# Kernel optimization log

Hardware: AMD Instinct MI355X
Metric: run time of the kernel (lower is better)

The kernel has to match this reference:

```python
import jax, jax.numpy as jnp
import numpy as np

N = 50000      # nodes
E = 800000     # edges
G = 1024       # graphs in batch
D_IN = 9       # atom feature dim
D = 64         # embedding_size


def _lin(k, fan_in, shape):
    s = 1.0 / np.sqrt(fan_in)
    return jax.random.uniform(k, shape, jnp.float32, -s, s)


def setup_inputs() -> dict:
    key = jax.random.key(0)
    ks = jax.random.split(key, 12)
    x = jax.random.normal(ks[0], (N, D_IN), dtype=jnp.float32)
    edge_index = jax.random.randint(ks[1], (2, E), 0, N, dtype=jnp.int32)
    # node -> graph id, sorted, every graph non-empty
    batch = (jnp.arange(N) * G // N).astype(jnp.int32)
    W0 = _lin(ks[2], D_IN, (D_IN, D)); b0 = _lin(ks[3], D_IN, (D,))
    W1 = _lin(ks[4], D, (D, D));       b1 = _lin(ks[5], D, (D,))
    W2 = _lin(ks[6], D, (D, D));       b2 = _lin(ks[7], D, (D,))
    W3 = _lin(ks[8], D, (D, D));       b3 = _lin(ks[9], D, (D,))
    Wout = _lin(ks[10], 2 * D, (2 * D, 1)); bout = _lin(ks[11], 2 * D, (1,))
    return {"x": x, "edge_index": edge_index, "batch": batch,
            "W0": W0, "b0": b0, "W1": W1, "b1": b1,
            "W2": W2, "b2": b2, "W3": W3, "b3": b3,
            "Wout": Wout, "bout": bout}


def reference(x, edge_index, batch, W0, b0, W1, b1, W2, b2, W3, b3, Wout, bout):
    n = x.shape[0]
    # GCNConv: add self-loops, symmetric normalization D^-1/2 (A+I) D^-1/2
    loops = jnp.arange(n, dtype=edge_index.dtype)
    row = jnp.concatenate([edge_index[0], loops])  # source
    col = jnp.concatenate([edge_index[1], loops])  # destination
    deg = jax.ops.segment_sum(jnp.ones_like(col, dtype=x.dtype), col, num_segments=n)
    dinv = jax.lax.rsqrt(deg)  # deg >= 1 thanks to self-loops
    norm = dinv[row] * dinv[col]  # [E+N]

    def conv(h, W, b):
        h = h @ W                               # [N, D]
        msg = norm[:, None] * h[row]            # [E+N, D]
        return jax.ops.segment_sum(msg, col, num_segments=n) + b

    h = jnp.tanh(conv(x, W0, b0))
    h = jnp.tanh(conv(h, W1, b1))
    h = jnp.tanh(conv(h, W2, b2))
    h = jnp.tanh(conv(h, W3, b3))
    # dropout is identity in eval mode
    gmax = jax.ops.segment_max(h, batch, num_segments=G)                       # [G, D]
    cnt = jax.ops.segment_sum(jnp.ones((n, 1), h.dtype), batch, num_segments=G)
    gmean = jax.ops.segment_sum(h, batch, num_segments=G) / jnp.maximum(cnt, 1.0)
    pooled = jnp.concatenate([gmax, gmean], axis=1)                            # [G, 2D]
    return pooled @ Wout + bout
```

## Files before the change

### kernel.cpp

```cpp
#include <hip/hip_runtime.h>
#include <hip/hip_fp16.h>
#include <math.h>

#define N_NODES 50000
#define N_EDGES 800000
#define N_GRAPHS 1024
#define DIM 64
#define PAD 64
#define ZROW N_NODES


__global__ void deg_fill(const int* __restrict__ row, const int* __restrict__ col,
                         int* __restrict__ ideg, int* __restrict__ esrc_pad) {
    int e = blockIdx.x * 256 + threadIdx.x;
    if (e >= N_EDGES) return;
    int r = row[e];
    int c = col[e];
    int rank = atomicAdd(&ideg[c], 1);
    if (rank < PAD) esrc_pad[c * PAD + rank] = r;
}


__global__ void gemm9(const float* __restrict__ x, const float* __restrict__ W,
                      const int* __restrict__ ideg, __half* __restrict__ th) {
    __shared__ float Wl[9 * DIM];
    int tid = threadIdx.x;
    for (int i = tid; i < 9 * DIM; i += 256) Wl[i] = W[i];
    __syncthreads();
    int node = blockIdx.x * 4 + (tid >> 6);
    int d = tid & 63;
    if (node >= N_NODES) return;
    const float* xr = x + (size_t)node * 9;
    float acc = 0.0f;
#pragma unroll
    for (int k = 0; k < 9; ++k) acc += xr[k] * Wl[k * DIM + d];
    float dv = rsqrtf((float)ideg[node] + 1.0f);
    th[(size_t)node * DIM + d] = __float2half(dv * acc);
}

__global__ void gemm64(const float* __restrict__ h, const float* __restrict__ W,
                       const int* __restrict__ ideg, uint2* __restrict__ th2) {
    __shared__ float At[64][68];
    __shared__ float Bl[64][68];
    int tid = threadIdx.x;
    int n0 = blockIdx.x * 64;

    {
        const float4* W4 = (const float4*)W;
#pragma unroll
        for (int i = 0; i < 4; ++i) {
            int idx = tid + 256 * i;
            int k = idx >> 4;
            int d4 = idx & 15;
            float4 v = W4[idx];
            *(float4*)&Bl[k][d4 * 4] = v;
        }
    }
    {
        int node = tid >> 2;
        int seg = tid & 3;
        int gn = n0 + node;
        bool ok = gn < N_NODES;
        const float4* h4 = (const float4*)h;
#pragma unroll
        for (int i = 0; i < 4; ++i) {
            int c4 = seg * 4 + i;
            float4 v = ok ? h4[(size_t)gn * 16 + c4] : make_float4(0.f, 0.f, 0.f, 0.f);
            int d = c4 * 4;
            At[d + 0][node] = v.x;
            At[d + 1][node] = v.y;
            At[d + 2][node] = v.z;
            At[d + 3][node] = v.w;
        }
    }
    __syncthreads();

    int ty = tid >> 4;
    int tx = tid & 15;
    float c00 = 0, c01 = 0, c02 = 0, c03 = 0;
    float c10 = 0, c11 = 0, c12 = 0, c13 = 0;
    float c20 = 0, c21 = 0, c22 = 0, c23 = 0;
    float c30 = 0, c31 = 0, c32 = 0, c33 = 0;
#pragma unroll 8
    for (int k = 0; k < 64; ++k) {
        float4 a = *(const float4*)&At[k][ty * 4];
        float4 b = *(const float4*)&Bl[k][tx * 4];
        c00 += a.x * b.x; c01 += a.x * b.y; c02 += a.x * b.z; c03 += a.x * b.w;
        c10 += a.y * b.x; c11 += a.y * b.y; c12 += a.y * b.z; c13 += a.y * b.w;
        c20 += a.z * b.x; c21 += a.z * b.y; c22 += a.z * b.z; c23 += a.z * b.w;
        c30 += a.w * b.x; c31 += a.w * b.y; c32 += a.w * b.z; c33 += a.w * b.w;
    }
    int gn = n0 + ty * 4;
#define STORE_ROW(r, CA, CB, CC, CD)                                          \
    if (gn + r < N_NODES) {                                                   \
        float dv = rsqrtf((float)ideg[gn + r] + 1.0f);                        \
        __half2 p0 = __floats2half2_rn(dv * CA, dv * CB);                     \
        __half2 p1 = __floats2half2_rn(dv * CC, dv * CD);                     \
        uint2 o;                                                              \
        o.x = *(unsigned*)&p0;                                                \
        o.y = *(unsigned*)&p1;                                                \
        th2[(size_t)(gn + r) * 16 + tx] = o;                                  \
    }
    STORE_ROW(0, c00, c01, c02, c03)
    STORE_ROW(1, c10, c11, c12, c13)
    STORE_ROW(2, c20, c21, c22, c23)
    STORE_ROW(3, c30, c31, c32, c33)
#undef STORE_ROW
}


__device__ __forceinline__ float4 h4tof4(uint2 v) {
    __half2 a = *reinterpret_cast<const __half2*>(&v.x);
    __half2 c = *reinterpret_cast<const __half2*>(&v.y);
    float2 fa = __half22float2(a);
    float2 fc = __half22float2(c);
    return make_float4(fa.x, fa.y, fc.x, fc.y);
}

__device__ __forceinline__ void add4(float4& a, const float4& r) {
    a.x += r.x; a.y += r.y; a.z += r.z; a.w += r.w;
}

__device__ __forceinline__ void fold4(float4& a, int m) {
    a.x += __shfl_xor(a.x, m, 64);
    a.y += __shfl_xor(a.y, m, 64);
    a.z += __shfl_xor(a.z, m, 64);
    a.w += __shfl_xor(a.w, m, 64);
}

__global__ void gather_tanh(const int* __restrict__ esrc_pad, const int* __restrict__ ideg,
                            const uint2* __restrict__ th2, const float* __restrict__ b,
                            float4* __restrict__ hout4) {
    int tid = threadIdx.x;
    int wid = tid >> 6;
    int lane = tid & 63;
    int sub = lane & 15;
    int grp = lane >> 4;
    int nodeA = blockIdx.x * 8 + wid * 2;
    int nodeB = nodeA + 1;

    int degA = min(ideg[nodeA], PAD);
    int degB = min(ideg[nodeB], PAD);
    int sA = nodeA * PAD, sB = nodeB * PAD;
    int eA = sA + degA, eB = sB + degB;

    float4 accA = make_float4(0.f, 0.f, 0.f, 0.f);
    float4 accB = make_float4(0.f, 0.f, 0.f, 0.f);

    if (grp == 0) add4(accA, h4tof4(th2[(size_t)nodeA * 16 + sub]));
    else if (grp == 1) add4(accB, h4tof4(th2[(size_t)nodeB * 16 + sub]));

    int iters = max((degA + 15) >> 4, (degB + 15) >> 4);
    int jA = sA + grp, jB = sB + grp;

    for (int it = 0; it < iters; ++it) {
        bool vA0 = jA + 0 < eA, vA1 = jA + 4 < eA, vA2 = jA + 8 < eA, vA3 = jA + 12 < eA;
        bool vB0 = jB + 0 < eB, vB1 = jB + 4 < eB, vB2 = jB + 8 < eB, vB3 = jB + 12 < eB;
        int a0 = esrc_pad[vA0 ? jA + 0 : 0], a1 = esrc_pad[vA1 ? jA + 4 : 0];
        int a2 = esrc_pad[vA2 ? jA + 8 : 0], a3 = esrc_pad[vA3 ? jA + 12 : 0];
        int b0 = esrc_pad[vB0 ? jB + 0 : 0], b1 = esrc_pad[vB1 ? jB + 4 : 0];
        int b2 = esrc_pad[vB2 ? jB + 8 : 0], b3 = esrc_pad[vB3 ? jB + 12 : 0];
        a0 = vA0 ? a0 : ZROW; a1 = vA1 ? a1 : ZROW; a2 = vA2 ? a2 : ZROW; a3 = vA3 ? a3 : ZROW;
        b0 = vB0 ? b0 : ZROW; b1 = vB1 ? b1 : ZROW; b2 = vB2 ? b2 : ZROW; b3 = vB3 ? b3 : ZROW;
        uint2 rA0 = th2[(size_t)a0 * 16 + sub];
        uint2 rA1 = th2[(size_t)a1 * 16 + sub];
        uint2 rA2 = th2[(size_t)a2 * 16 + sub];
        uint2 rA3 = th2[(size_t)a3 * 16 + sub];
        uint2 rB0 = th2[(size_t)b0 * 16 + sub];
        uint2 rB1 = th2[(size_t)b1 * 16 + sub];
        uint2 rB2 = th2[(size_t)b2 * 16 + sub];
        uint2 rB3 = th2[(size_t)b3 * 16 + sub];
        add4(accA, h4tof4(rA0)); add4(accA, h4tof4(rA1));
        add4(accA, h4tof4(rA2)); add4(accA, h4tof4(rA3));
        add4(accB, h4tof4(rB0)); add4(accB, h4tof4(rB1));
        add4(accB, h4tof4(rB2)); add4(accB, h4tof4(rB3));
        jA += 16; jB += 16;
    }

    fold4(accA, 16);
    fold4(accA, 32);
    fold4(accB, 16);
    fold4(accB, 32);

    float4 bv = ((const float4*)b)[sub];
    float dvA = rsqrtf((float)degA + 1.0f);
    float dvB = rsqrtf((float)degB + 1.0f);
    float dv = (grp == 1) ? dvB : dvA;
    float4 res = (grp == 1) ? accB : accA;
    res.x = tanhf(dv * res.x + bv.x);
    res.y = tanhf(dv * res.y + bv.y);
    res.z = tanhf(dv * res.z + bv.z);
    res.w = tanhf(dv * res.w + bv.w);
    if (grp == 0) hout4[(size_t)nodeA * 16 + sub] = res;
    else if (grp == 1) hout4[(size_t)nodeB * 16 + sub] = res;
}


__device__ __forceinline__ int lower_bound(const int* a, int n, int key) {
    int lo = 0, hi = n;
    while (lo < hi) {
        int mid = (lo + hi) >> 1;
        if (a[mid] < key) lo = mid + 1; else hi = mid;
    }
    return lo;
}

__global__ void pool_out(const float* __restrict__ h, const int* __restrict__ batch,
                         const float* __restrict__ Wout, const float* __restrict__ bout,
                         float* __restrict__ out) {
    __shared__ float smax[4][DIM];
    __shared__ float ssum[4][DIM];
    __shared__ int bounds[2];
    int g = blockIdx.x;
    int tid = threadIdx.x, w = tid >> 6, d = tid & 63;
    if (tid == 0) {
        bounds[0] = lower_bound(batch, N_NODES, g);
        bounds[1] = lower_bound(batch, N_NODES, g + 1);
    }
    __syncthreads();
    int start = bounds[0], end = bounds[1];
    float mx = -INFINITY, sum = 0.0f;
    for (int n = start + w; n < end; n += 4) {
        float v = h[(size_t)n * DIM + d];
        mx = fmaxf(mx, v);
        sum += v;
    }
    smax[w][d] = mx;
    ssum[w][d] = sum;
    __syncthreads();
    if (w == 0) {
        mx = fmaxf(fmaxf(smax[0][d], smax[1][d]), fmaxf(smax[2][d], smax[3][d]));
        sum = ssum[0][d] + ssum[1][d] + ssum[2][d] + ssum[3][d];
        float cnt = (float)(end - start);
        float mean = sum / fmaxf(cnt, 1.0f);
        float v = mx * Wout[d] + mean * Wout[DIM + d];
#pragma unroll
        for (int off = 32; off > 0; off >>= 1) v += __shfl_down(v, off, 64);
        if (d == 0) out[g] = v + bout[0];
    }
}


static inline size_t align256(size_t x) { return (x + 255) & ~(size_t)255; }

extern "C" void kernel_launch(void* const* d_in, const int* in_sizes, int n_in,
                              void* d_out, int out_size, void* d_ws, size_t ws_size,
                              hipStream_t stream) {
    const float* x     = (const float*)d_in[0];
    const int*   ei    = (const int*)d_in[1];
    const int*   batch = (const int*)d_in[2];
    const float* W0    = (const float*)d_in[3];
    const float* b0    = (const float*)d_in[4];
    const float* W1    = (const float*)d_in[5];
    const float* b1    = (const float*)d_in[6];
    const float* W2    = (const float*)d_in[7];
    const float* b2    = (const float*)d_in[8];
    const float* W3    = (const float*)d_in[9];
    const float* b3    = (const float*)d_in[10];
    const float* Wout  = (const float*)d_in[11];
    const float* bout  = (const float*)d_in[12];
    float* out = (float*)d_out;

    const int* row = ei;
    const int* col = ei + N_EDGES;

    char* ws = (char*)d_ws;
    size_t off = 0;
    int*    ideg     = (int*)(ws + off);    off += align256((size_t)N_NODES * 4);
    int*    esrc_pad = (int*)(ws + off);    off += align256((size_t)N_NODES * PAD * 4);
    __half* th       = (__half*)(ws + off); off += align256(((size_t)N_NODES + 1) * DIM * 2);
    float*  hA       = (float*)(ws + off);  off += align256((size_t)N_NODES * DIM * 4);
    (void)ws_size;

    const int edge_blocks = (N_EDGES + 255) / 256;
    const int wave_blocks = N_NODES / 4;
    const int gath_blocks = N_NODES / 8;
    const int gemm_blocks = (N_NODES + 63) / 64;

    hipMemsetAsync(ideg, 0, (size_t)N_NODES * 4, stream);
    hipMemsetAsync(th + (size_t)ZROW * DIM, 0, DIM * 2, stream);
    deg_fill<<<edge_blocks, 256, 0, stream>>>(row, col, ideg, esrc_pad);

    gemm9<<<wave_blocks, 256, 0, stream>>>(x, W0, ideg, th);
    gather_tanh<<<gath_blocks, 256, 0, stream>>>(esrc_pad, ideg, (const uint2*)th, b0, (float4*)hA);

    const float* Ws[3] = {W1, W2, W3};
    const float* bs[3] = {b1, b2, b3};
    for (int l = 0; l < 3; ++l) {
        gemm64<<<gemm_blocks, 256, 0, stream>>>(hA, Ws[l], ideg, (uint2*)th);
        gather_tanh<<<gath_blocks, 256, 0, stream>>>(esrc_pad, ideg, (const uint2*)th, bs[l], (float4*)hA);
    }

    pool_out<<<N_GRAPHS, 256, 0, stream>>>(hA, batch, Wout, bout, out);
    (void)out_size; (void)n_in; (void)in_sizes;
}
```

Before: 280.6 us.

## Partition degree fill by destination slice and gather one node per quarter-wave

The degree/adjacency fill now runs 8 groups of blocks, each scanning all edges but handling only destinations in its node slice. The intent is to localise atomics and scattered writes to an L2-resident slice, at the cost of reading the column array 8 times. The gather kernel now assigns one node per 16-lane group instead of two nodes per wave. It loads neighbour indices as int4 vectors, issues 16 independent row loads per step into four accumulators, and drops the cross-lane shuffle reduction. This should raise memory-level parallelism, but lanes within a wave may diverge on loop trip count when neighbour degrees differ.

Result: faster. 274.8 us, median of 2 (-2.1%).

```diff
diff --git a/kernel.cpp b/kernel.cpp
--- a/kernel.cpp
+++ b/kernel.cpp
@@ -8,16 +8,22 @@
 #define DIM 64
 #define PAD 64
 #define ZROW N_NODES
+#define SLICE 6250
+#define QBLK 208
 
 
 __global__ void deg_fill(const int* __restrict__ row, const int* __restrict__ col,
                          int* __restrict__ ideg, int* __restrict__ esrc_pad) {
-    int e = blockIdx.x * 256 + threadIdx.x;
-    if (e >= N_EDGES) return;
-    int r = row[e];
-    int c = col[e];
-    int rank = atomicAdd(&ideg[c], 1);
-    if (rank < PAD) esrc_pad[c * PAD + rank] = r;
+    int slice = blockIdx.x & 7;
+    int q = blockIdx.x >> 3;
+    int lo = slice * SLICE, hi = lo + SLICE;
+    for (int e = q * 256 + threadIdx.x; e < N_EDGES; e += QBLK * 256) {
+        int c = col[e];
+        if (c >= lo && c < hi) {
+            int rank = atomicAdd(&ideg[c], 1);
+            if (rank < PAD) esrc_pad[c * PAD + rank] = row[e];
+        }
+    }
 }
 
 
@@ -121,13 +127,6 @@
     a.x += r.x; a.y += r.y; a.z += r.z; a.w += r.w;
 }
 
-__device__ __forceinline__ void fold4(float4& a, int m) {
-    a.x += __shfl_xor(a.x, m, 64);
-    a.y += __shfl_xor(a.y, m, 64);
-    a.z += __shfl_xor(a.z, m, 64);
-    a.w += __shfl_xor(a.w, m, 64);
-}
-
 __global__ void gather_tanh(const int* __restrict__ esrc_pad, const int* __restrict__ ideg,
                             const uint2* __restrict__ th2, const float* __restrict__ b,
                             float4* __restrict__ hout4) {
@@ -136,63 +135,54 @@
     int lane = tid & 63;
     int sub = lane & 15;
     int grp = lane >> 4;
-    int nodeA = blockIdx.x * 8 + wid * 2;
-    int nodeB = nodeA + 1;
-
-    int degA = min(ideg[nodeA], PAD);
-    int degB = min(ideg[nodeB], PAD);
-    int sA = nodeA * PAD, sB = nodeB * PAD;
-    int eA = sA + degA, eB = sB + degB;
-
-    float4 accA = make_float4(0.f, 0.f, 0.f, 0.f);
-    float4 accB = make_float4(0.f, 0.f, 0.f, 0.f);
-
-    if (grp == 0) add4(accA, h4tof4(th2[(size_t)nodeA * 16 + sub]));
-    else if (grp == 1) add4(accB, h4tof4(th2[(size_t)nodeB * 16 + sub]));
-
-    int iters = max((degA + 15) >> 4, (degB + 15) >> 4);
-    int jA = sA + grp, jB = sB + grp;
-
-    for (int it = 0; it < iters; ++it) {
-        bool vA0 = jA + 0 < eA, vA1 = jA + 4 < eA, vA2 = jA + 8 < eA, vA3 = jA + 12 < eA;
-        bool vB0 = jB + 0 < eB, vB1 = jB + 4 < eB, vB2 = jB + 8 < eB, vB3 = jB + 12 < eB;
-        int a0 = esrc_pad[vA0 ? jA + 0 : 0], a1 = esrc_pad[vA1 ? jA + 4 : 0];
-        int a2 = esrc_pad[vA2 ? jA + 8 : 0], a3 = esrc_pad[vA3 ? jA + 12 : 0];
-        int b0 = esrc_pad[vB0 ? jB + 0 : 0], b1 = esrc_pad[vB1 ? jB + 4 : 0];
-        int b2 = esrc_pad[vB2 ? jB + 8 : 0], b3 = esrc_pad[vB3 ? jB + 12 : 0];
-        a0 = vA0 ? a0 : ZROW; a1 = vA1 ? a1 : ZROW; a2 = vA2 ? a2 : ZROW; a3 = vA3 ? a3 : ZROW;
-        b0 = vB0 ? b0 : ZROW; b1 = vB1 ? b1 : ZROW; b2 = vB2 ? b2 : ZROW; b3 = vB3 ? b3 : ZROW;
-        uint2 rA0 = th2[(size_t)a0 * 16 + sub];
-        uint2 rA1 = th2[(size_t)a1 * 16 + sub];
-        uint2 rA2 = th2[(size_t)a2 * 16 + sub];
-        uint2 rA3 = th2[(size_t)a3 * 16 + sub];
-        uint2 rB0 = th2[(size_t)b0 * 16 + sub];
-        uint2 rB1 = th2[(size_t)b1 * 16 + sub];
-        uint2 rB2 = th2[(size_t)b2 * 16 + sub];
-        uint2 rB3 = th2[(size_t)b3 * 16 + sub];
-        add4(accA, h4tof4(rA0)); add4(accA, h4tof4(rA1));
-        add4(accA, h4tof4(rA2)); add4(accA, h4tof4(rA3));
-        add4(accB, h4tof4(rB0)); add4(accB, h4tof4(rB1));
-        add4(accB, h4tof4(rB2)); add4(accB, h4tof4(rB3));
-        jA += 16; jB += 16;
-    }
-
-    fold4(accA, 16);
-    fold4(accA, 32);
-    fold4(accB, 16);
-    fold4(accB, 32);
+    int node = blockIdx.x * 16 + wid * 4 + grp;
+
+    int deg = min(ideg[node], PAD);
+    const int* ep = esrc_pad + node * PAD;
+
+    float4 acc0 = h4tof4(th2[(size_t)node * 16 + sub]);
+    float4 acc1 = make_float4(0.f, 0.f, 0.f, 0.f);
+    float4 acc2 = make_float4(0.f, 0.f, 0.f, 0.f);
+    float4 acc3 = make_float4(0.f, 0.f, 0.f, 0.f);
+
+    for (int base = 0; base < deg; base += 16) {
+        int4 i0 = *(const int4*)(ep + base + 0);
+        int4 i1 = *(const int4*)(ep + base + 4);
+        int4 i2 = *(const int4*)(ep + base + 8);
+        int4 i3 = *(const int4*)(ep + base + 12);
+        int idx[16] = {i0.x, i0.y, i0.z, i0.w, i1.x, i1.y, i1.z, i1.w,
+                       i2.x, i2.y, i2.z, i2.w, i3.x, i3.y, i3.z, i3.w};
+        int rem = deg - base;
+        uint2 r[16];
+#pragma unroll
+        for (int j = 0; j < 16; ++j) {
+            int s = (j < rem) ? idx[j] : ZROW;
+            r[j] = th2[(size_t)s * 16 + sub];
+        }
+#pragma unroll
+        for (int j = 0; j < 16; ++j) {
+            float4 v = h4tof4(r[j]);
+            if ((j & 3) == 0) add4(acc0, v);
+            else if ((j & 3) == 1) add4(acc1, v);
+            else if ((j & 3) == 2) add4(acc2, v);
+            else add4(acc3, v);
+        }
+    }
+
+    float4 acc;
+    acc.x = (acc0.x + acc1.x) + (acc2.x + acc3.x);
+    acc.y = (acc0.y + acc1.y) + (acc2.y + acc3.y);
+    acc.z = (acc0.z + acc1.z) + (acc2.z + acc3.z);
+    acc.w = (acc0.w + acc1.w) + (acc2.w + acc3.w);
 
     float4 bv = ((const float4*)b)[sub];
-    float dvA = rsqrtf((float)degA + 1.0f);
-    float dvB = rsqrtf((float)degB + 1.0f);
-    float dv = (grp == 1) ? dvB : dvA;
-    float4 res = (grp == 1) ? accB : accA;
-    res.x = tanhf(dv * res.x + bv.x);
-    res.y = tanhf(dv * res.y + bv.y);
-    res.z = tanhf(dv * res.z + bv.z);
-    res.w = tanhf(dv * res.w + bv.w);
-    if (grp == 0) hout4[(size_t)nodeA * 16 + sub] = res;
-    else if (grp == 1) hout4[(size_t)nodeB * 16 + sub] = res;
+    float dv = rsqrtf((float)deg + 1.0f);
+    float4 res;
+    res.x = tanhf(dv * acc.x + bv.x);
+    res.y = tanhf(dv * acc.y + bv.y);
+    res.z = tanhf(dv * acc.z + bv.z);
+    res.w = tanhf(dv * acc.w + bv.w);
+    hout4[(size_t)node * 16 + sub] = res;
 }
 
 
@@ -272,14 +262,13 @@
     float*  hA       = (float*)(ws + off);  off += align256((size_t)N_NODES * DIM * 4);
     (void)ws_size;
 
-    const int edge_blocks = (N_EDGES + 255) / 256;
     const int wave_blocks = N_NODES / 4;
-    const int gath_blocks = N_NODES / 8;
+    const int gath_blocks = N_NODES / 16;
     const int gemm_blocks = (N_NODES + 63) / 64;
 
     hipMemsetAsync(ideg, 0, (size_t)N_NODES * 4, stream);
     hipMemsetAsync(th + (size_t)ZROW * DIM, 0, DIM * 2, stream);
-    deg_fill<<<edge_blocks, 256, 0, stream>>>(row, col, ideg, esrc_pad);
+    deg_fill<<<8 * QBLK, 256, 0, stream>>>(row, col, ideg, esrc_pad);
 
     gemm9<<<wave_blocks, 256, 0, stream>>>(x, W0, ideg, th);
     gather_tanh<<<gath_blocks, 256, 0, stream>>>(esrc_pad, ideg, (const uint2*)th, b0, (float4*)hA);
```
